# Kernel optimization log

Measured on AMD Instinct MI355X. Metric: run time of the kernel, lower is better.

## Reference

```python
import jax, jax.numpy as jnp
import numpy as np

HEAD_NUM = 16

def setup_inputs() -> dict:
    key = jax.random.key(0)
    ks = jax.random.split(key, 5)
    B, N, D = 2, 2048, 1024
    x = jax.random.normal(ks[0], (B, N, D), dtype=jnp.float32)
    scale = 0.02
    W_q = jax.random.normal(ks[1], (D, D), dtype=jnp.float32) * scale
    W_k = jax.random.normal(ks[2], (D, D), dtype=jnp.float32) * scale
    W_v = jax.random.normal(ks[3], (D, D), dtype=jnp.float32) * scale
    W_o = jax.random.normal(ks[4], (D, D), dtype=jnp.float32) * scale
    return {"x": x, "W_q": W_q, "W_k": W_k, "W_v": W_v, "W_o": W_o}

def reference(x, W_q, W_k, W_v, W_o):
    B, N, D = x.shape
    H = HEAD_NUM
    hd = D // H  # head_dim
    inv_sqrt_hd = 1.0 / np.sqrt(hd).astype(np.float32)

    def split_head(t):
        # einops 'b n (d h) -> b h n d' : head index is the INNER factor
        return t.reshape(B, N, hd, H).transpose(0, 3, 1, 2)  # [B,H,N,hd]

    # nn.Linear(bias=False): y = x @ W.T
    Q = split_head(x @ W_q.T)
    K = split_head(x @ W_k.T)
    V = split_head(x @ W_v.T)

    scores = jnp.einsum('bhnd,bhmd->bhnm', Q, K) * inv_sqrt_hd  # [B,H,N,N]
    attn = jax.nn.softmax(scores, axis=-1)
    heads = jnp.einsum('bhnm,bhmd->bhnd', attn, V)  # [B,H,N,hd]

    # einops 'b h n d -> b n (h d)' : head index is the OUTER factor here
    concat = heads.transpose(0, 2, 1, 3).reshape(B, N, D)
    return concat @ W_o.T
```

## Files before the change

### kernel.cpp

```cpp
#include <hip/hip_runtime.h>
#include <hip/hip_bf16.h>

typedef __bf16 bf16_t;
typedef __attribute__((ext_vector_type(8))) __bf16 bf16x8;
typedef __attribute__((ext_vector_type(4))) __bf16 bf16x4;
typedef __attribute__((ext_vector_type(4))) float f32x4;
typedef __attribute__((ext_vector_type(16))) float f32x16;

#define MFMA16(A,B,C) __builtin_amdgcn_mfma_f32_16x16x32_bf16((A),(B),(C),0,0,0)
#define MFMA32(A,B,C) __builtin_amdgcn_mfma_f32_32x32x16_bf16((A),(B),(C),0,0,0)

#define BATCH 2
#define SEQ 2048
#define DMODEL 1024
#define NHEAD 16
#define HDIM 64
#define MROWS (BATCH * SEQ)

__device__ __forceinline__ void async16(const bf16_t* g, bf16_t* l) {
    __builtin_amdgcn_global_load_lds(
        (const __attribute__((address_space(1))) unsigned int*)g,
        (__attribute__((address_space(3))) unsigned int*)l, 16, 0, 0);
}

__device__ __forceinline__ bf16x8 ldsA32(const bf16_t* base, int row, int chunk) {
    return *(const bf16x8*)&base[row * 32 + ((chunk ^ ((row >> 1) & 3)) << 3)];
}
__device__ __forceinline__ bf16x8 ldsA64(const bf16_t* base, int row, int chunk) {
    return *(const bf16x8*)&base[row * 64 + ((chunk ^ (row & 7)) << 3)];
}
__device__ __forceinline__ bf16x8 ldsV(const bf16_t* base, int row, int lc) {
    int phys = (lc & 8) | ((lc & 7) ^ (row & 7));
    return *(const bf16x8*)&base[row * 128 + phys * 8];
}

__device__ __forceinline__ unsigned pk(float a, float b) {
    union { unsigned u; bf16_t h[2]; } t;
    t.h[0] = (bf16_t)a;
    t.h[1] = (bf16_t)b;
    return t.u;
}

__global__ void split_x_kernel(const float* __restrict__ src, bf16_t* __restrict__ hi,
                               int n4) {
    int i = blockIdx.x * 256 + threadIdx.x;
    if (i >= n4) return;
    f32x4 v = ((const f32x4*)src)[i];
    bf16x4 h;
#pragma unroll
    for (int c = 0; c < 4; ++c) h[c] = (bf16_t)v[c];
    ((bf16x4*)hi)[i] = h;
}

__global__ void split_w_kernel(const float* __restrict__ Wq, const float* __restrict__ Wk,
                               const float* __restrict__ Wv, const float* __restrict__ Wo,
                               bf16_t* __restrict__ hi, bf16_t* __restrict__ lo) {
    const int z = blockIdx.y;
    const float* src = (z == 0) ? Wq : (z == 1) ? Wk : (z == 2) ? Wv : Wo;
    const float scale = (z == 0) ? 0.125f * 1.44269504088896f : 1.0f;
    int i = blockIdx.x * 256 + threadIdx.x;
    int row = i >> 8, col4 = i & 255;
    int r_src;
    if (z < 3) {
        int h = row >> 6, d = row & 63;
        r_src = 16 * d + h;
    } else {
        r_src = row;
    }
    f32x4 v = ((const f32x4*)src)[r_src * 256 + col4];
    bf16x4 h4, l4;
#pragma unroll
    for (int c = 0; c < 4; ++c) {
        float val = v[c] * scale;
        bf16_t hh = (bf16_t)val;
        h4[c] = hh;
        l4[c] = (bf16_t)(val - (float)hh);
    }
    ((bf16x4*)(hi + (size_t)z * DMODEL * DMODEL))[i] = h4;
    if (z == 3) ((bf16x4*)lo)[i] = l4;
}

__global__ __launch_bounds__(256)
void gemm_qkv_kernel(const bf16_t* __restrict__ Ah, const bf16_t* __restrict__ Bh0,
                     bf16_t* __restrict__ Coh0, int M, int Nn, int Kk) {
    __shared__ __align__(16) bf16_t smem[2][8192];

    const int z = blockIdx.z;
    const bf16_t* Bh = Bh0 + (size_t)z * Nn * Kk;
    const int m0 = blockIdx.y * 128, n0 = blockIdx.x * 128;
    const int tid = threadIdx.x;
    const int wave = tid >> 6, lane = tid & 63, lq = lane >> 4, ln = lane & 15;
    const int wr = wave >> 1, wc = wave & 1;

    const bf16_t* g_ptr[4];
    int l_off[4];
#pragma unroll
    for (int q = 0; q < 4; ++q) {
        int e = wave * 4 + q;
        int a = e >> 3, u = e & 7;
        int C = u * 64 + lane;
        int r = C >> 2, p = C & 3;
        int c = p ^ ((r >> 1) & 3);
        g_ptr[q] = (a == 0 ? Ah + (size_t)(m0 + r) * Kk
                           : Bh + (size_t)(n0 + r) * Kk) + c * 8;
        l_off[q] = a * 4096 + u * 512;
    }

    f32x4 acc[4][4] = {};

#pragma unroll
    for (int q = 0; q < 4; ++q)
        async16(g_ptr[q], &smem[0][l_off[q]]);

    const int NIT = Kk / 32;
    for (int j = 0; j < NIT; ++j) {
        __syncthreads();
        if (j + 1 < NIT) {
#pragma unroll
            for (int q = 0; q < 4; ++q)
                async16(g_ptr[q] + (j + 1) * 32, &smem[(j + 1) & 1][l_off[q]]);
        }
        const bf16_t* cur = smem[j & 1];

        bf16x8 ah[4], bh[4];
#pragma unroll
        for (int t = 0; t < 4; ++t) {
            ah[t] = ldsA32(cur, wr * 64 + t * 16 + ln, lq);
            bh[t] = ldsA32(cur + 4096, wc * 64 + t * 16 + ln, lq);
        }
#pragma unroll
        for (int tm = 0; tm < 4; ++tm)
#pragma unroll
            for (int tn = 0; tn < 4; ++tn)
                acc[tm][tn] = MFMA16(ah[tm], bh[tn], acc[tm][tn]);
    }

#pragma unroll
    for (int tm = 0; tm < 4; ++tm)
#pragma unroll
        for (int tn = 0; tn < 4; ++tn)
#pragma unroll
            for (int p = 0; p < 4; ++p) {
                int gm = m0 + wr * 64 + tm * 16 + lq * 4 + p;
                int gn = n0 + wc * 64 + tn * 16 + ln;
                Coh0[(size_t)z * M * Nn + (size_t)gm * Nn + gn] =
                    (bf16_t)acc[tm][tn][p];
            }
}

__global__ __launch_bounds__(256)
void gemm_out_kernel(const bf16_t* __restrict__ Ah,
                     const bf16_t* __restrict__ Bh, const bf16_t* __restrict__ Bl,
                     float* __restrict__ Cf, int M, int Nn, int Kk) {
    __shared__ __align__(16) bf16_t smem[2][10240];

    const int m0 = blockIdx.y * 64, n0 = blockIdx.x * 128;
    const int tid = threadIdx.x;
    const int wave = tid >> 6, lane = tid & 63, lq = lane >> 4, ln = lane & 15;
    const int wr = wave >> 1, wc = wave & 1;

    const bf16_t* g_ptr[5];
    int l_off[5];
#pragma unroll
    for (int q = 0; q < 5; ++q) {
        int e = wave * 5 + q;
        const bf16_t* arr;
        int u, rowbase, lb;
        if (e < 4)       { arr = Ah; u = e;      rowbase = m0; lb = 0; }
        else if (e < 12) { arr = Bh; u = e - 4;  rowbase = n0; lb = 2048; }
        else             { arr = Bl; u = e - 12; rowbase = n0; lb = 6144; }
        int r = u * 16 + (lane >> 2), p = lane & 3;
        int c = p ^ ((r >> 1) & 3);
        g_ptr[q] = arr + (size_t)(rowbase + r) * Kk + c * 8;
        l_off[q] = lb + u * 512;
    }

    f32x4 acc[2][4] = {};

#pragma unroll
    for (int q = 0; q < 5; ++q)
        async16(g_ptr[q], &smem[0][l_off[q]]);

    const int NIT = Kk / 32;
    for (int j = 0; j < NIT; ++j) {
        __syncthreads();
        if (j + 1 < NIT) {
#pragma unroll
            for (int q = 0; q < 5; ++q)
                async16(g_ptr[q] + (j + 1) * 32, &smem[(j + 1) & 1][l_off[q]]);
        }
        const bf16_t* cur = smem[j & 1];

        bf16x8 ah[2], bh[4], bl[4];
#pragma unroll
        for (int t = 0; t < 2; ++t)
            ah[t] = ldsA32(cur, wr * 32 + t * 16 + ln, lq);
#pragma unroll
        for (int t = 0; t < 4; ++t) {
            bh[t] = ldsA32(cur + 2048, wc * 64 + t * 16 + ln, lq);
            bl[t] = ldsA32(cur + 6144, wc * 64 + t * 16 + ln, lq);
        }
#pragma unroll
        for (int tm = 0; tm < 2; ++tm)
#pragma unroll
            for (int tn = 0; tn < 4; ++tn) {
                acc[tm][tn] = MFMA16(ah[tm], bh[tn], acc[tm][tn]);
                acc[tm][tn] = MFMA16(ah[tm], bl[tn], acc[tm][tn]);
            }
    }

#pragma unroll
    for (int tm = 0; tm < 2; ++tm)
#pragma unroll
        for (int tn = 0; tn < 4; ++tn)
#pragma unroll
            for (int p = 0; p < 4; ++p) {
                int gm = m0 + wr * 32 + tm * 16 + lq * 4 + p;
                int gn = n0 + wc * 64 + tn * 16 + ln;
                Cf[(size_t)gm * Nn + gn] = acc[tm][tn][p];
            }
}

__global__ __launch_bounds__(256)
void vtrans_kernel(const bf16_t* __restrict__ Vn, bf16_t* __restrict__ Vt) {
    __shared__ bf16_t t[64][66];
    const int bh = blockIdx.y;
    const int b = bh >> 4, h = bh & 15;
    const int n0 = blockIdx.x * 64;
    const int tid = threadIdx.x;
#pragma unroll
    for (int it = 0; it < 2; ++it) {
        int c = it * 256 + tid;
        int r = c >> 3, p = c & 7;
        *(bf16x8*)&t[r][p * 8] =
            *(const bf16x8*)&Vn[((size_t)(b * SEQ + n0 + r)) * DMODEL + h * HDIM + p * 8];
    }
    __syncthreads();
#pragma unroll
    for (int it = 0; it < 2; ++it) {
        int c = it * 256 + tid;
        int d = c >> 3, p = c & 7;
        bf16x8 v;
#pragma unroll
        for (int e = 0; e < 8; ++e) v[e] = t[p * 8 + e][d];
        *(bf16x8*)&Vt[((size_t)(bh * HDIM + d)) * SEQ + n0 + p * 8] = v;
    }
}

__global__ __launch_bounds__(256)
void attn_kernel(const bf16_t* __restrict__ Qh, const bf16_t* __restrict__ Kh,
                 const bf16_t* __restrict__ Vt, bf16_t* __restrict__ Ch) {
    __shared__ __align__(16) bf16_t smem[2][16384];

    const int bh = blockIdx.y;
    const int b = bh >> 4, h = bh & 15;
    const int q0 = blockIdx.x * 128;
    const int tid = threadIdx.x;
    const int wave = tid >> 6, lane = tid & 63;
    const int ln32 = lane & 31, hl = lane >> 5;

    bf16x8 qfh[4];
    {
        size_t qrow = ((size_t)(b * SEQ + q0 + wave * 32 + ln32)) * DMODEL +
                      h * HDIM + hl * 8;
#pragma unroll
        for (int c = 0; c < 4; ++c)
            qfh[c] = *(const bf16x8*)&Qh[qrow + c * 16];
    }

    const bf16_t* g_base[8];
    int l_off[8];
    size_t g_step[8];
#pragma unroll
    for (int q = 0; q < 8; ++q) {
        int e = wave * 8 + q;
        if (e < 16) {
            int u = e;
            int r = u * 8 + (lane >> 3), p = lane & 7;
            int c = p ^ (r & 7);
            g_base[q] = Kh + ((size_t)(b * SEQ + r)) * DMODEL + h * HDIM + c * 8;
            l_off[q] = u * 512;
            g_step[q] = (size_t)128 * DMODEL;
        } else {
            int u = e - 16;
            int r = u * 4 + (lane >> 4), c16 = lane & 15;
            int lc = (c16 & 8) | ((c16 & 7) ^ (r & 7));
            g_base[q] = Vt + ((size_t)(bh * HDIM + r)) * SEQ + lc * 8;
            l_off[q] = 8192 + u * 512;
            g_step[q] = 128;
        }
    }

    f32x16 o[2];
#pragma unroll
    for (int dt = 0; dt < 2; ++dt)
#pragma unroll
        for (int r = 0; r < 16; ++r) o[dt][r] = 0.0f;
    float rs = 0.0f;

#pragma unroll
    for (int q = 0; q < 8; ++q)
        async16(g_base[q], &smem[0][l_off[q]]);

    for (int j = 0; j < 16; ++j) {
        __syncthreads();
        if (j < 15) {
#pragma unroll
            for (int q = 0; q < 8; ++q)
                async16(g_base[q] + (j + 1) * g_step[q],
                        &smem[(j + 1) & 1][l_off[q]]);
        }
        const bf16_t* Kc = smem[j & 1];
        const bf16_t* Vc = smem[j & 1] + 8192;

#pragma unroll
        for (int kt = 0; kt < 4; ++kt) {
            f32x16 st;
#pragma unroll
            for (int r = 0; r < 16; ++r) st[r] = 0.0f;
#pragma unroll
            for (int c = 0; c < 4; ++c) {
                bf16x8 kh = ldsA64(Kc, kt * 32 + ln32, 2 * c + hl);
                st = MFMA32(kh, qfh[c], st);
            }
            float pexp[16];
#pragma unroll
            for (int r = 0; r < 16; ++r) {
                pexp[r] = __builtin_amdgcn_exp2f(st[r]);
                rs += pexp[r];
            }
            bf16x8 pfrag[2];
#pragma unroll
            for (int s1 = 0; s1 < 2; ++s1) {
                unsigned lo01 = pk(pexp[8 * s1 + 0], pexp[8 * s1 + 1]);
                unsigned lo23 = pk(pexp[8 * s1 + 2], pexp[8 * s1 + 3]);
                unsigned hi01 = pk(pexp[8 * s1 + 4], pexp[8 * s1 + 5]);
                unsigned hi23 = pk(pexp[8 * s1 + 6], pexp[8 * s1 + 7]);
                unsigned sa = hl ? lo01 : hi01;
                unsigned sb = hl ? lo23 : hi23;
                unsigned ra = (unsigned)__shfl_xor((int)sa, 32);
                unsigned rb = (unsigned)__shfl_xor((int)sb, 32);
                union { bf16x8 v; unsigned u[4]; } outv;
                outv.u[0] = hl ? ra : lo01;
                outv.u[1] = hl ? rb : lo23;
                outv.u[2] = hl ? hi01 : ra;
                outv.u[3] = hl ? hi23 : rb;
                pfrag[s1] = outv.v;
            }
#pragma unroll
            for (int dt = 0; dt < 2; ++dt)
#pragma unroll
                for (int s1 = 0; s1 < 2; ++s1) {
                    int sg = kt * 2 + s1;
                    bf16x8 va = ldsV(Vc, dt * 32 + ln32, 2 * sg + hl);
                    o[dt] = MFMA32(va, pfrag[s1], o[dt]);
                }
        }
    }

    rs += __shfl_xor(rs, 32);
    float inv = 1.0f / rs;

    float* fbuf = (float*)&smem[0][0];
#pragma unroll
    for (int dh = 0; dh < 2; ++dh) {
        __syncthreads();
#pragma unroll
        for (int r = 0; r < 16; ++r) {
            int d_loc = (r & 3) + 8 * (r >> 2) + 4 * hl;
            fbuf[wave * 1056 + ln32 * 33 + d_loc] = o[dh][r] * inv;
        }
        __syncthreads();
#pragma unroll
        for (int qq = 0; qq < 16; ++qq) {
            int qrow = hl * 16 + qq;
            float v = fbuf[wave * 1056 + qrow * 33 + ln32];
            size_t gidx = ((size_t)(b * SEQ + q0 + wave * 32 + qrow)) * DMODEL +
                          h * HDIM + dh * 32 + ln32;
            Ch[gidx] = (bf16_t)v;
        }
    }
}

extern "C" void kernel_launch(void* const* d_in, const int* in_sizes, int n_in,
                              void* d_out, int out_size, void* d_ws, size_t ws_size,
                              hipStream_t stream) {
    const float* x  = (const float*)d_in[0];
    const float* Wq = (const float*)d_in[1];
    const float* Wk = (const float*)d_in[2];
    const float* Wv = (const float*)d_in[3];
    const float* Wo = (const float*)d_in[4];
    float* out = (float*)d_out;

    char* ws = (char*)d_ws;
    size_t off = 0;
    auto alloc = [&](size_t bytes) -> bf16_t* {
        bf16_t* p = (bf16_t*)(ws + off);
        off += (bytes + 255) & ~(size_t)255;
        return p;
    };
    const size_t XE = (size_t)MROWS * DMODEL;
    const size_t WE = (size_t)DMODEL * DMODEL;

    bf16_t* xh  = alloc(XE * 2);
    bf16_t* wh  = alloc(4 * WE * 2);
    bf16_t* wl  = alloc(WE * 2);
    bf16_t* qnh = alloc(3 * XE * 2);
    bf16_t* vth = alloc(XE * 2);
    bf16_t* ch  = alloc(XE * 2);
    (void)ws_size; (void)in_sizes; (void)n_in; (void)out_size;

    split_x_kernel<<<(int)(XE / 4 / 256), 256, 0, stream>>>(x, xh, (int)(XE / 4));
    split_w_kernel<<<dim3(WE / 4 / 256, 4), 256, 0, stream>>>(Wq, Wk, Wv, Wo, wh, wl);

    gemm_qkv_kernel<<<dim3(DMODEL / 128, MROWS / 128, 3), 256, 0, stream>>>(
        xh, wh, qnh, MROWS, DMODEL, DMODEL);

    vtrans_kernel<<<dim3(SEQ / 64, BATCH * NHEAD), 256, 0, stream>>>(qnh + 2 * XE, vth);

    attn_kernel<<<dim3(SEQ / 128, BATCH * NHEAD), 256, 0, stream>>>(
        qnh, qnh + XE, vth, ch);

    gemm_out_kernel<<<dim3(DMODEL / 128, MROWS / 64), 256, 0, stream>>>(
        ch, wh + 3 * WE, wl, out, MROWS, DMODEL, DMODEL);
}
```

Before: 198.2 us.

## Split attention KV range across two wave groups and merge split conversion kernels

The attention kernel now runs 512 threads per block, with two groups of four waves each processing half of the key/value sequence in 64-key tiles. Their partial outputs and row sums are combined through shared memory before normalisation and store. This aims to raise per-block parallelism and latency hiding in the attention loop, at the cost of an extra reduction pass and more synchronisation. Separately, the x and weight conversion kernels are fused into a single launch to cut launch overhead.

```diff
diff --git a/kernel.cpp b/kernel.cpp
--- a/kernel.cpp
+++ b/kernel.cpp
@@ -29,10 +29,6 @@
 __device__ __forceinline__ bf16x8 ldsA64(const bf16_t* base, int row, int chunk) {
     return *(const bf16x8*)&base[row * 64 + ((chunk ^ (row & 7)) << 3)];
 }
-__device__ __forceinline__ bf16x8 ldsV(const bf16_t* base, int row, int lc) {
-    int phys = (lc & 8) | ((lc & 7) ^ (row & 7));
-    return *(const bf16x8*)&base[row * 128 + phys * 8];
-}
 
 __device__ __forceinline__ unsigned pk(float a, float b) {
     union { unsigned u; bf16_t h[2]; } t;
@@ -41,24 +37,25 @@
     return t.u;
 }
 
-__global__ void split_x_kernel(const float* __restrict__ src, bf16_t* __restrict__ hi,
-                               int n4) {
-    int i = blockIdx.x * 256 + threadIdx.x;
-    if (i >= n4) return;
-    f32x4 v = ((const f32x4*)src)[i];
-    bf16x4 h;
-#pragma unroll
-    for (int c = 0; c < 4; ++c) h[c] = (bf16_t)v[c];
-    ((bf16x4*)hi)[i] = h;
-}
-
-__global__ void split_w_kernel(const float* __restrict__ Wq, const float* __restrict__ Wk,
-                               const float* __restrict__ Wv, const float* __restrict__ Wo,
-                               bf16_t* __restrict__ hi, bf16_t* __restrict__ lo) {
-    const int z = blockIdx.y;
+__global__ void split_kernel(const float* __restrict__ x, const float* __restrict__ Wq,
+                             const float* __restrict__ Wk, const float* __restrict__ Wv,
+                             const float* __restrict__ Wo, bf16_t* __restrict__ xh,
+                             bf16_t* __restrict__ wh, bf16_t* __restrict__ wl) {
+    int blk = blockIdx.x;
+    if (blk < 4096) {
+        int i = blk * 256 + threadIdx.x;
+        f32x4 v = ((const f32x4*)x)[i];
+        bf16x4 h;
+#pragma unroll
+        for (int c = 0; c < 4; ++c) h[c] = (bf16_t)v[c];
+        ((bf16x4*)xh)[i] = h;
+        return;
+    }
+    int e = blk - 4096;
+    int z = e >> 10;
+    int i = (e & 1023) * 256 + threadIdx.x;
     const float* src = (z == 0) ? Wq : (z == 1) ? Wk : (z == 2) ? Wv : Wo;
     const float scale = (z == 0) ? 0.125f * 1.44269504088896f : 1.0f;
-    int i = blockIdx.x * 256 + threadIdx.x;
     int row = i >> 8, col4 = i & 255;
     int r_src;
     if (z < 3) {
@@ -76,8 +73,8 @@
         h4[c] = hh;
         l4[c] = (bf16_t)(val - (float)hh);
     }
-    ((bf16x4*)(hi + (size_t)z * DMODEL * DMODEL))[i] = h4;
-    if (z == 3) ((bf16x4*)lo)[i] = l4;
+    ((bf16x4*)(wh + (size_t)z * DMODEL * DMODEL))[i] = h4;
+    if (z == 3) ((bf16x4*)wl)[i] = l4;
 }
 
 __global__ __launch_bounds__(256)
@@ -247,47 +244,48 @@
     }
 }
 
-__global__ __launch_bounds__(256)
+__global__ __launch_bounds__(512, 4)
 void attn_kernel(const bf16_t* __restrict__ Qh, const bf16_t* __restrict__ Kh,
                  const bf16_t* __restrict__ Vt, bf16_t* __restrict__ Ch) {
-    __shared__ __align__(16) bf16_t smem[2][16384];
+    __shared__ __align__(16) bf16_t smem[2][2][8192];
 
     const int bh = blockIdx.y;
     const int b = bh >> 4, h = bh & 15;
     const int q0 = blockIdx.x * 128;
     const int tid = threadIdx.x;
-    const int wave = tid >> 6, lane = tid & 63;
+    const int g = tid >> 8;
+    const int wv = (tid >> 6) & 3;
+    const int lane = tid & 63;
     const int ln32 = lane & 31, hl = lane >> 5;
 
     bf16x8 qfh[4];
     {
-        size_t qrow = ((size_t)(b * SEQ + q0 + wave * 32 + ln32)) * DMODEL +
+        size_t qrow = ((size_t)(b * SEQ + q0 + wv * 32 + ln32)) * DMODEL +
                       h * HDIM + hl * 8;
 #pragma unroll
         for (int c = 0; c < 4; ++c)
             qfh[c] = *(const bf16x8*)&Qh[qrow + c * 16];
     }
 
-    const bf16_t* g_base[8];
-    int l_off[8];
-    size_t g_step[8];
-#pragma unroll
-    for (int q = 0; q < 8; ++q) {
-        int e = wave * 8 + q;
-        if (e < 16) {
-            int u = e;
-            int r = u * 8 + (lane >> 3), p = lane & 7;
-            int c = p ^ (r & 7);
-            g_base[q] = Kh + ((size_t)(b * SEQ + r)) * DMODEL + h * HDIM + c * 8;
+    bf16_t* gsm = &smem[g][0][0];
+    const bf16_t* g_base[4];
+    int l_off[4];
+    size_t g_step[4];
+#pragma unroll
+    for (int q = 0; q < 4; ++q) {
+        int e = wv * 4 + q;
+        int a = e >> 3, u = e & 7;
+        int r = u * 8 + (lane >> 3), p = lane & 7;
+        int c = p ^ (r & 7);
+        if (a == 0) {
+            g_base[q] = Kh + ((size_t)(b * SEQ + g * 1024 + r)) * DMODEL +
+                        h * HDIM + c * 8;
             l_off[q] = u * 512;
-            g_step[q] = (size_t)128 * DMODEL;
+            g_step[q] = (size_t)64 * DMODEL;
         } else {
-            int u = e - 16;
-            int r = u * 4 + (lane >> 4), c16 = lane & 15;
-            int lc = (c16 & 8) | ((c16 & 7) ^ (r & 7));
-            g_base[q] = Vt + ((size_t)(bh * HDIM + r)) * SEQ + lc * 8;
-            l_off[q] = 8192 + u * 512;
-            g_step[q] = 128;
+            g_base[q] = Vt + ((size_t)(bh * HDIM + r)) * SEQ + g * 1024 + c * 8;
+            l_off[q] = 4096 + u * 512;
+            g_step[q] = 64;
         }
     }
 
@@ -299,22 +297,23 @@
     float rs = 0.0f;
 
 #pragma unroll
-    for (int q = 0; q < 8; ++q)
-        async16(g_base[q], &smem[0][l_off[q]]);
+    for (int q = 0; q < 4; ++q)
+        async16(g_base[q], gsm + l_off[q]);
 
     for (int j = 0; j < 16; ++j) {
         __syncthreads();
         if (j < 15) {
 #pragma unroll
-            for (int q = 0; q < 8; ++q)
+            for (int q = 0; q < 4; ++q)
                 async16(g_base[q] + (j + 1) * g_step[q],
-                        &smem[(j + 1) & 1][l_off[q]]);
-        }
-        const bf16_t* Kc = smem[j & 1];
-        const bf16_t* Vc = smem[j & 1] + 8192;
-
-#pragma unroll
-        for (int kt = 0; kt < 4; ++kt) {
+                        gsm + ((j + 1) & 1) * 8192 + l_off[q]);
+        }
+        const bf16_t* Kc = gsm + (j & 1) * 8192;
+        const bf16_t* Vc = Kc + 4096;
+
+        bf16x8 pfrag[4];
+#pragma unroll
+        for (int kt = 0; kt < 2; ++kt) {
             f32x16 st;
 #pragma unroll
             for (int r = 0; r < 16; ++r) st[r] = 0.0f;
@@ -329,7 +328,6 @@
                 pexp[r] = __builtin_amdgcn_exp2f(st[r]);
                 rs += pexp[r];
             }
-            bf16x8 pfrag[2];
 #pragma unroll
             for (int s1 = 0; s1 < 2; ++s1) {
                 unsigned lo01 = pk(pexp[8 * s1 + 0], pexp[8 * s1 + 1]);
@@ -345,37 +343,65 @@
                 outv.u[1] = hl ? rb : lo23;
                 outv.u[2] = hl ? hi01 : ra;
                 outv.u[3] = hl ? hi23 : rb;
-                pfrag[s1] = outv.v;
-            }
-#pragma unroll
-            for (int dt = 0; dt < 2; ++dt)
-#pragma unroll
-                for (int s1 = 0; s1 < 2; ++s1) {
-                    int sg = kt * 2 + s1;
-                    bf16x8 va = ldsV(Vc, dt * 32 + ln32, 2 * sg + hl);
-                    o[dt] = MFMA32(va, pfrag[s1], o[dt]);
-                }
-        }
+                pfrag[kt * 2 + s1] = outv.v;
+            }
+        }
+#pragma unroll
+        for (int dt = 0; dt < 2; ++dt)
+#pragma unroll
+            for (int s = 0; s < 4; ++s) {
+                bf16x8 va = ldsA64(Vc, dt * 32 + ln32, 2 * s + hl);
+                o[dt] = MFMA32(va, pfrag[s], o[dt]);
+            }
     }
 
     rs += __shfl_xor(rs, 32);
-    float inv = 1.0f / rs;
-
-    float* fbuf = (float*)&smem[0][0];
-#pragma unroll
-    for (int dh = 0; dh < 2; ++dh) {
-        __syncthreads();
-#pragma unroll
-        for (int r = 0; r < 16; ++r) {
-            int d_loc = (r & 3) + 8 * (r >> 2) + 4 * hl;
-            fbuf[wave * 1056 + ln32 * 33 + d_loc] = o[dh][r] * inv;
-        }
-        __syncthreads();
+
+    __syncthreads();
+    float* cbuf = (float*)smem;
+    float* rbuf = cbuf + 8192;
+    if (g == 1) {
+#pragma unroll
+        for (int dt = 0; dt < 2; ++dt)
+#pragma unroll
+            for (int r = 0; r < 16; ++r) {
+                int d = dt * 32 + (r & 3) + 8 * (r >> 2) + 4 * hl;
+                cbuf[d * 128 + wv * 32 + ln32] = o[dt][r];
+            }
+        if (hl == 0) rbuf[wv * 32 + ln32] = rs;
+    }
+    __syncthreads();
+    float inv = 0.0f;
+    if (g == 0) {
+#pragma unroll
+        for (int dt = 0; dt < 2; ++dt)
+#pragma unroll
+            for (int r = 0; r < 16; ++r) {
+                int d = dt * 32 + (r & 3) + 8 * (r >> 2) + 4 * hl;
+                o[dt][r] += cbuf[d * 128 + wv * 32 + ln32];
+            }
+        inv = 1.0f / (rs + rbuf[wv * 32 + ln32]);
+    }
+    __syncthreads();
+    float* fbuf = (float*)smem;
+    if (g == 0) {
+#pragma unroll
+        for (int dh = 0; dh < 2; ++dh)
+#pragma unroll
+            for (int r = 0; r < 16; ++r) {
+                int d_loc = (r & 3) + 8 * (r >> 2) + 4 * hl;
+                fbuf[dh * 4224 + wv * 1056 + ln32 * 33 + d_loc] = o[dh][r] * inv;
+            }
+    }
+    __syncthreads();
+    {
+        int gw = tid >> 6;
+        int dh = gw >> 2, w = gw & 3;
 #pragma unroll
         for (int qq = 0; qq < 16; ++qq) {
             int qrow = hl * 16 + qq;
-            float v = fbuf[wave * 1056 + qrow * 33 + ln32];
-            size_t gidx = ((size_t)(b * SEQ + q0 + wave * 32 + qrow)) * DMODEL +
+            float v = fbuf[dh * 4224 + w * 1056 + qrow * 33 + ln32];
+            size_t gidx = ((size_t)(b * SEQ + q0 + w * 32 + qrow)) * DMODEL +
                           h * HDIM + dh * 32 + ln32;
             Ch[gidx] = (bf16_t)v;
         }
@@ -410,15 +436,14 @@
     bf16_t* ch  = alloc(XE * 2);
     (void)ws_size; (void)in_sizes; (void)n_in; (void)out_size;
 
-    split_x_kernel<<<(int)(XE / 4 / 256), 256, 0, stream>>>(x, xh, (int)(XE / 4));
-    split_w_kernel<<<dim3(WE / 4 / 256, 4), 256, 0, stream>>>(Wq, Wk, Wv, Wo, wh, wl);
+    split_kernel<<<8192, 256, 0, stream>>>(x, Wq, Wk, Wv, Wo, xh, wh, wl);
 
     gemm_qkv_kernel<<<dim3(DMODEL / 128, MROWS / 128, 3), 256, 0, stream>>>(
         xh, wh, qnh, MROWS, DMODEL, DMODEL);
 
     vtrans_kernel<<<dim3(SEQ / 64, BATCH * NHEAD), 256, 0, stream>>>(qnh + 2 * XE, vth);
 
-    attn_kernel<<<dim3(SEQ / 128, BATCH * NHEAD), 256, 0, stream>>>(
+    attn_kernel<<<dim3(SEQ / 128, BATCH * NHEAD), 512, 0, stream>>>(
         qnh, qnh + XE, vth, ch);
 
     gemm_out_kernel<<<dim3(DMODEL / 128, MROWS / 64), 256, 0, stream>>>(
```

Result: faster. 193.2 us (-2.5%).
